# Kernel tuning notes

Measured on AMD Instinct MI355X. Metric: run time of the kernel, lower is better.

The kernel has to match this reference:

```python
import jax, jax.numpy as jnp
import numpy as np

P = 0.3            # swap probability (matches init_kwargs p)
H = 224
W = 224
PERM_SEED = 42     # fixed key so the reference is deterministic


def _index_permute(key, h, w, p):
    """Sequential random-neighbor swap permutation over an h*w grid.

    Faithful to CLOPLayer._index_permute: visit all flat indices in a random
    order; for each, with prob p swap it with one of its 4 toroidal neighbors
    (each with prob p/4). Implemented as a lax.scan over the visitation order
    (the swaps are inherently sequential / order-dependent).
    """
    n = h * w
    k1, k2 = jax.random.split(key)
    order = jax.random.permutation(k1, n)                       # visitation order
    probs = jnp.array([1.0 - p, p / 4, p / 4, p / 4, p / 4], dtype=jnp.float32)
    rs = jax.random.choice(k2, 5, shape=(n,), p=probs)          # move type per step

    def step(indexes, inp):
        idx, r = inp
        i = idx // w
        j = idx % w
        ip = jnp.where(r == 1, (i + 1) % h, jnp.where(r == 2, (i - 1) % h, i))
        jp = jnp.where(r == 3, (j + 1) % w, jnp.where(r == 4, (j - 1) % w, j))
        idx2 = jnp.where(r == 0, idx, ip * w + jp)              # r==0 -> self-swap (no-op)
        a = indexes[idx]
        b = indexes[idx2]
        indexes = indexes.at[idx].set(b).at[idx2].set(a)
        return indexes, None

    indexes = jnp.arange(n, dtype=jnp.int32)
    indexes, _ = jax.lax.scan(step, indexes, (order.astype(jnp.int32), rs.astype(jnp.int32)))
    return indexes


def setup_inputs() -> dict:
    key = jax.random.key(0)
    x = jax.random.normal(key, (128, 3, H, W), dtype=jnp.float32)
    return {"x": x}


def reference(x) -> jnp.ndarray:
    b, c, h, w = x.shape
    idx = _index_permute(jax.random.key(PERM_SEED), h, w, P)     # [h*w] int32
    flat = x.reshape(b, c, h * w)
    # torch.gather(flat, 2, idx broadcast over b,c) == take along last axis
    res = jnp.take(flat, idx, axis=2)
    return res.reshape(b, c, h, w)
```

## Files before the change

kernel.cpp:

```cpp
#include <hip/hip_runtime.h>
#include <cstdint>
#include <cstring>
#include <vector>
#include <algorithm>


#define PH 224
#define PW 224
#define PN (PH * PW)
#define NBC (128 * 3)

#define R_OUT 56
#define HALO 8
#define S_ROWS (R_OUT + 2 * HALO)
#define NWIN (PH / R_OUT)
#define KWIN (R_OUT * PW)

typedef float f4v __attribute__((ext_vector_type(4)));
typedef unsigned short u4v __attribute__((ext_vector_type(4)));

static inline uint32_t rotl32(uint32_t v, int d) {
  return (v << d) | (v >> (32 - d));
}

static void tf2x32(uint32_t k0, uint32_t k1, uint32_t x0, uint32_t x1,
                   uint32_t& o0, uint32_t& o1) {
  const uint32_t ks0 = k0, ks1 = k1, ks2 = k0 ^ k1 ^ 0x1BD11BDAu;
  uint32_t v0 = x0 + ks0;
  uint32_t v1 = x1 + ks1;
  static const int ra[4] = {13, 15, 26, 6};
  static const int rb[4] = {17, 29, 16, 24};
#define R4X(rr)                             \
  do {                                      \
    for (int _i = 0; _i < 4; ++_i) {        \
      v0 += v1;                             \
      v1 = rotl32(v1, (rr)[_i]);            \
      v1 ^= v0;                             \
    }                                       \
  } while (0)
  R4X(ra); v0 += ks1; v1 += ks2 + 1u;
  R4X(rb); v0 += ks2; v1 += ks0 + 2u;
  R4X(ra); v0 += ks0; v1 += ks1 + 3u;
  R4X(rb); v0 += ks1; v1 += ks2 + 4u;
  R4X(ra); v0 += ks2; v1 += ks0 + 5u;
#undef R4X
  o0 = v0;
  o1 = v1;
}

static void jax_split2(uint32_t k0, uint32_t k1,
                       uint32_t& a0, uint32_t& a1, uint32_t& b0, uint32_t& b1) {
  tf2x32(k0, k1, 0u, 0u, a0, a1);
  tf2x32(k0, k1, 0u, 1u, b0, b1);
}

static inline uint32_t jax_rb32(uint32_t k0, uint32_t k1, uint32_t i) {
  uint32_t y0, y1;
  tf2x32(k0, k1, 0u, i, y0, y1);
  return y0 ^ y1;
}

static std::vector<int> compute_perm() {
  const int n = PN;
  const uint32_t K0 = 0u, K1 = 42u;

  uint32_t k1a, k1b, k2a, k2b;
  jax_split2(K0, K1, k1a, k1b, k2a, k2b);

  std::vector<int> order(n);
  for (int i = 0; i < n; ++i) order[i] = i;
  uint32_t ck0 = k1a, ck1 = k1b;
  std::vector<std::pair<uint32_t, int>> kv(n);
  for (int round = 0; round < 2; ++round) {
    uint32_t nk0, nk1, sk0, sk1;
    jax_split2(ck0, ck1, nk0, nk1, sk0, sk1);
    ck0 = nk0; ck1 = nk1;
    for (int i = 0; i < n; ++i) {
      kv[i] = {jax_rb32(sk0, sk1, (uint32_t)i), order[i]};
    }
    std::stable_sort(kv.begin(), kv.end(),
                     [](const std::pair<uint32_t, int>& a,
                        const std::pair<uint32_t, int>& b) {
                       return a.first < b.first;
                     });
    for (int i = 0; i < n; ++i) order[i] = kv[i].second;
  }

  float probs[5] = {(float)(1.0 - 0.3), (float)(0.3 / 4), (float)(0.3 / 4),
                    (float)(0.3 / 4), (float)(0.3 / 4)};
  float pc[5];
  pc[0] = probs[0];
  for (int i = 1; i < 5; ++i) pc[i] = pc[i - 1] + probs[i];

  std::vector<uint8_t> rs(n);
  for (int i = 0; i < n; ++i) {
    uint32_t bits = jax_rb32(k2a, k2b, (uint32_t)i);
    uint32_t fb = (bits >> 9) | 0x3f800000u;
    float u;
    std::memcpy(&u, &fb, 4);
    u -= 1.0f;
    if (u < 0.0f) u = 0.0f;
    float r = pc[4] * (1.0f - u);
    int ind = (int)(std::lower_bound(pc, pc + 5, r) - pc);
    rs[i] = (uint8_t)ind;
  }

  std::vector<int> idx(n);
  for (int i = 0; i < n; ++i) idx[i] = i;
  for (int t = 0; t < n; ++t) {
    const int id = order[t];
    const int r = rs[t];
    const int i = id / PW, j = id % PW;
    int ip = i, jp = j;
    if (r == 1)      ip = (i + 1) % PH;
    else if (r == 2) ip = (i - 1 + PH) % PH;
    else if (r == 3) jp = (j + 1) % PW;
    else if (r == 4) jp = (j - 1 + PW) % PW;
    const int id2 = (r == 0) ? id : (ip * PW + jp);
    const int a = idx[id];
    const int b = idx[id2];
    idx[id]  = b;
    idx[id2] = a;
  }
  return idx;
}

struct PermHolder {
  std::vector<int> h_idx;
  std::vector<uint16_t> h_lofs;
  int* d_idx = nullptr;
  uint16_t* d_lofs = nullptr;
  bool lds_ok = false;

  PermHolder() {
    h_idx = compute_perm();

    h_lofs.assign((size_t)NWIN * KWIN, 0);
    bool ok = true;
    for (int w = 0; w < NWIN && ok; ++w) {
      const int g0 = w * R_OUT - HALO;
      for (int kk = 0; kk < KWIN; ++kk) {
        const int k = w * KWIN + kk;
        const int s = h_idx[k];
        const int srow = s / PW, scol = s % PW;
        int i = ((srow - g0) % PH + PH) % PH;
        if (i >= S_ROWS) { ok = false; break; }
        h_lofs[(size_t)w * KWIN + kk] = (uint16_t)(i * PW + scol);
      }
    }

    int* p = nullptr;
    if (hipMalloc(&p, PN * sizeof(int)) == hipSuccess &&
        hipMemcpy(p, h_idx.data(), PN * sizeof(int),
                  hipMemcpyHostToDevice) == hipSuccess) {
      d_idx = p;
    }
    if (ok) {
      uint16_t* q = nullptr;
      if (hipMalloc(&q, (size_t)NWIN * KWIN * sizeof(uint16_t)) == hipSuccess &&
          hipMemcpy(q, h_lofs.data(), (size_t)NWIN * KWIN * sizeof(uint16_t),
                    hipMemcpyHostToDevice) == hipSuccess) {
        d_lofs = q;
        lds_ok = true;
      }
    }
  }
};
static PermHolder g_perm;

__global__ __launch_bounds__(256) void clop_lds(
    const float* __restrict__ x, const uint16_t* __restrict__ lofs,
    float* __restrict__ out) {
  __shared__ float tile[S_ROWS * PW];

  const int w = blockIdx.x;
  const size_t bc = blockIdx.y;
  const int g0 = w * R_OUT - HALO;
  const float* xs = x + bc * PN;

  for (int t = threadIdx.x; t < S_ROWS * (PW / 4); t += 256) {
    const int i = t / (PW / 4);
    const int j = (t % (PW / 4)) * 4;
    int g = g0 + i;
    if (g < 0) g += PH;
    else if (g >= PH) g -= PH;
    const f4v v = *(const f4v*)(xs + g * PW + j);
    *(f4v*)(tile + i * PW + j) = v;
  }
  __syncthreads();

  const uint16_t* lw = lofs + (size_t)w * KWIN;
  float* ob = out + bc * PN + (size_t)w * KWIN;
  for (int t = threadIdx.x; t < KWIN / 4; t += 256) {
    const u4v o4 = *(const u4v*)(lw + t * 4);
    f4v v;
    v.x = tile[o4.x];
    v.y = tile[o4.y];
    v.z = tile[o4.z];
    v.w = tile[o4.w];
    __builtin_nontemporal_store(v, (f4v*)(ob + t * 4));
  }
}

__global__ __launch_bounds__(256) void clop_gather(
    const float* __restrict__ x, const int* __restrict__ idx,
    float* __restrict__ out) {
  const int k = blockIdx.x * 256 + threadIdx.x;
  const int s = idx[k];
  const size_t bc0 = (size_t)blockIdx.y * 8;
#pragma unroll
  for (int t = 0; t < 8; ++t) {
    const size_t bc = bc0 + t;
    out[bc * PN + k] = x[bc * PN + s];
  }
}

extern "C" void kernel_launch(void* const* d_in, const int* in_sizes, int n_in,
                              void* d_out, int out_size, void* d_ws,
                              size_t ws_size, hipStream_t stream) {
  const float* x = (const float*)d_in[0];
  float* out = (float*)d_out;

  if (g_perm.lds_ok) {
    dim3 grid(NWIN, NBC);
    clop_lds<<<grid, 256, 0, stream>>>(x, g_perm.d_lofs, out);
    return;
  }

  const int* idx;
  if (g_perm.d_idx != nullptr) {
    idx = g_perm.d_idx;
  } else {
    (void)hipMemcpyAsync(d_ws, g_perm.h_idx.data(), PN * sizeof(int),
                         hipMemcpyHostToDevice, stream);
    idx = (const int*)d_ws;
  }
  dim3 grid(PN / 256, NBC / 8);
  clop_gather<<<grid, 256, 0, stream>>>(x, idx, out);
}
```

Before: 153.4 us.

## Shrink LDS window, use 512-thread blocks, and prefetch offsets before staging

Reduces the output window from 56 to 32 rows so each block's LDS tile shrinks, allowing more resident blocks per CU, and doubles the block size to 512 threads. Staging and emit loops are fully unrolled with fixed trip counts, and the permutation offsets are loaded into registers before the tile staging so their latency overlaps the input loads. The trade-off is a larger halo fraction, meaning more redundant row reads per output row.

```diff
diff --git a/kernel.cpp b/kernel.cpp
--- a/kernel.cpp
+++ b/kernel.cpp
@@ -10,11 +10,14 @@
 #define PN (PH * PW)
 #define NBC (128 * 3)
 
-#define R_OUT 56
+#define R_OUT 32
 #define HALO 8
 #define S_ROWS (R_OUT + 2 * HALO)
 #define NWIN (PH / R_OUT)
 #define KWIN (R_OUT * PW)
+#define TPB 512
+#define STAGE_F4 (S_ROWS * (PW / 4))
+#define EMIT_F4 (KWIN / 4)
 
 typedef float f4v __attribute__((ext_vector_type(4)));
 typedef unsigned short u4v __attribute__((ext_vector_type(4)));
@@ -168,7 +171,7 @@
 };
 static PermHolder g_perm;
 
-__global__ __launch_bounds__(256) void clop_lds(
+__global__ __launch_bounds__(TPB) void clop_lds(
     const float* __restrict__ x, const uint16_t* __restrict__ lofs,
     float* __restrict__ out) {
   __shared__ float tile[S_ROWS * PW];
@@ -178,27 +181,40 @@
   const int g0 = w * R_OUT - HALO;
   const float* xs = x + bc * PN;
 
-  for (int t = threadIdx.x; t < S_ROWS * (PW / 4); t += 256) {
-    const int i = t / (PW / 4);
-    const int j = (t % (PW / 4)) * 4;
-    int g = g0 + i;
-    if (g < 0) g += PH;
-    else if (g >= PH) g -= PH;
-    const f4v v = *(const f4v*)(xs + g * PW + j);
-    *(f4v*)(tile + i * PW + j) = v;
+  const uint16_t* lw = lofs + (size_t)w * KWIN;
+  u4v o4[4];
+#pragma unroll
+  for (int i = 0; i < 4; ++i) {
+    const int t = (int)threadIdx.x + i * TPB;
+    if (t < EMIT_F4) o4[i] = *(const u4v*)(lw + t * 4);
+  }
+
+#pragma unroll
+  for (int i = 0; i < 6; ++i) {
+    const int t = (int)threadIdx.x + i * TPB;
+    if (t < STAGE_F4) {
+      const int r = t / (PW / 4);
+      const int j = (t % (PW / 4)) * 4;
+      int g = g0 + r;
+      if (g < 0) g += PH;
+      else if (g >= PH) g -= PH;
+      *(f4v*)(tile + r * PW + j) = *(const f4v*)(xs + g * PW + j);
+    }
   }
   __syncthreads();
 
-  const uint16_t* lw = lofs + (size_t)w * KWIN;
   float* ob = out + bc * PN + (size_t)w * KWIN;
-  for (int t = threadIdx.x; t < KWIN / 4; t += 256) {
-    const u4v o4 = *(const u4v*)(lw + t * 4);
-    f4v v;
-    v.x = tile[o4.x];
-    v.y = tile[o4.y];
-    v.z = tile[o4.z];
-    v.w = tile[o4.w];
-    __builtin_nontemporal_store(v, (f4v*)(ob + t * 4));
+#pragma unroll
+  for (int i = 0; i < 4; ++i) {
+    const int t = (int)threadIdx.x + i * TPB;
+    if (t < EMIT_F4) {
+      f4v v;
+      v.x = tile[o4[i].x];
+      v.y = tile[o4[i].y];
+      v.z = tile[o4[i].z];
+      v.w = tile[o4[i].w];
+      __builtin_nontemporal_store(v, (f4v*)(ob + t * 4));
+    }
   }
 }
 
@@ -223,7 +239,7 @@
 
   if (g_perm.lds_ok) {
     dim3 grid(NWIN, NBC);
-    clop_lds<<<grid, 256, 0, stream>>>(x, g_perm.d_lofs, out);
+    clop_lds<<<grid, TPB, 0, stream>>>(x, g_perm.d_lofs, out);
     return;
   }
 
```

New measurement: 133.9 us. 1.15x faster.
